# Kernel optimization log

Hardware: AMD Instinct MI355X
Metric: run time of the kernel (lower is better)

Reference implementation:

```python
import jax, jax.numpy as jnp
from jax import lax
import numpy as np

DN = ('NCHW', 'OIHW', 'NCHW')


def _conv(x, w, b, stride):
    y = lax.conv_general_dilated(x, w, (stride, stride), 'VALID', dimension_numbers=DN)
    return jax.nn.relu(y + b[None, :, None, None])


def setup_inputs() -> dict:
    key = jax.random.key(0)
    ks = jax.random.split(key, 24)
    B = 1024
    s = 0.05
    inp = {
        'rgb_image': jax.random.normal(ks[0], (B, 15000), jnp.float32),
        'distance': jax.random.uniform(ks[1], (B,), jnp.float32),
        'speed': jax.random.uniform(ks[2], (B,), jnp.float32),
        # LaneFollower (PilotNet-style CNN) params
        'conv1_w': s * jax.random.normal(ks[3], (24, 1, 5, 5), jnp.float32),
        'conv1_b': jnp.zeros((24,), jnp.float32),
        'conv2_w': s * jax.random.normal(ks[4], (36, 24, 5, 5), jnp.float32),
        'conv2_b': jnp.zeros((36,), jnp.float32),
        'conv3_w': s * jax.random.normal(ks[5], (48, 36, 5, 5), jnp.float32),
        'conv3_b': jnp.zeros((48,), jnp.float32),
        'conv4_w': s * jax.random.normal(ks[6], (64, 48, 3, 3), jnp.float32),
        'conv4_b': jnp.zeros((64,), jnp.float32),
        'fc1_w': s * jax.random.normal(ks[7], (5120, 100), jnp.float32),
        'fc1_b': jnp.zeros((100,), jnp.float32),
        'fc2_w': s * jax.random.normal(ks[8], (100, 50), jnp.float32),
        'fc2_b': jnp.zeros((50,), jnp.float32),
        'fc3_w': s * jax.random.normal(ks[9], (50, 10), jnp.float32),
        'fc3_b': jnp.zeros((10,), jnp.float32),
        'fc4_w': s * jax.random.normal(ks[10], (10, 1), jnp.float32),
        'fc4_b': jnp.zeros((1,), jnp.float32),
        # AEBS MLP params: 3 -> 12 -> 24 -> 4
        'a1_w': s * jax.random.normal(ks[11], (3, 12), jnp.float32),
        'a1_b': jnp.zeros((12,), jnp.float32),
        'a2_w': s * jax.random.normal(ks[12], (12, 24), jnp.float32),
        'a2_b': jnp.zeros((24,), jnp.float32),
        'a3_w': s * jax.random.normal(ks[13], (24, 4), jnp.float32),
        'a3_b': jnp.zeros((4,), jnp.float32),
    }
    return inp


def reference(rgb_image, distance, speed,
              conv1_w, conv1_b, conv2_w, conv2_b, conv3_w, conv3_b, conv4_w, conv4_b,
              fc1_w, fc1_b, fc2_w, fc2_b, fc3_w, fc3_b, fc4_w, fc4_b,
              a1_w, a1_b, a2_w, a2_b, a3_w, a3_b):
    B = rgb_image.shape[0]
    # lane_follow_input[i, j] = 1 if flat[i + j*200] > 0 else 0  ==> transpose of (75,200) reshape
    x = jnp.where(rgb_image.reshape(B, 75, 200) > 0, 1.0, 0.0).transpose(0, 2, 1)
    x = x[:, None, :, :]  # [B,1,200,75]
    x = _conv(x, conv1_w, conv1_b, 2)  # [B,24,98,36]
    x = _conv(x, conv2_w, conv2_b, 2)  # [B,36,47,16]
    x = _conv(x, conv3_w, conv3_b, 2)  # [B,48,22,6]
    x = _conv(x, conv4_w, conv4_b, 1)  # [B,64,20,4]
    x = x.reshape(B, -1)  # [B,5120]
    x = jax.nn.relu(x @ fc1_w + fc1_b)
    x = jax.nn.relu(x @ fc2_w + fc2_b)
    x = jax.nn.relu(x @ fc3_w + fc3_b)
    steering = (x @ fc4_w + fc4_b)[:, 0]  # [B]
    steering = lax.stop_gradient(steering)  # torch.no_grad() on lane follower
    aebs_in = jnp.stack([steering, distance, speed], axis=-1)  # [B,3]
    h = jax.nn.relu(aebs_in @ a1_w + a1_b)
    h = jax.nn.relu(h @ a2_w + a2_b)
    brake_force = h @ a3_w + a3_b  # [B,4]
    return brake_force
```

## Files before the change

### kernel.cpp

```cpp
#include <hip/hip_runtime.h>

typedef _Float16 f16;
typedef _Float16 f16x4 __attribute__((ext_vector_type(4)));
typedef _Float16 f16x8 __attribute__((ext_vector_type(8)));
typedef float f32x4 __attribute__((ext_vector_type(4)));

__global__ __launch_bounds__(256) void repack1m_k(f16* __restrict__ dst, const float* __restrict__ src){
  int idx = blockIdx.x*256 + threadIdx.x;
  if (idx >= 1024) return;
  int i = idx & 7, l = (idx >> 3) & 63, mt = idx >> 9;
  int co = mt*16 + (l & 15);
  int k = (l >> 4)*8 + i;
  f16 v = (f16)0.0f;
  if (co < 24 && k < 25){
    int kw = k / 5, kh = k - kw*5;
    v = (f16)src[co*25 + kh*5 + kw];
  }
  dst[idx] = v;
}
__global__ __launch_bounds__(256) void repack2c_k(f16* __restrict__ dst, const float* __restrict__ src){
  for (int idx = blockIdx.x*256 + threadIdx.x; idx < 29184; idx += gridDim.x*256){
    int i = idx & 7, l = (idx >> 3) & 63, rest = idx >> 9;
    int mt = rest % 3, s = rest / 3;
    int co = mt*16 + (l & 15);
    int k = s*32 + (l >> 4)*8 + i;
    f16 v = (f16)0.0f;
    if (co < 36 && k < 600){
      int tap = k / 24, ci = k - tap*24;
      v = (f16)src[(co*24 + ci)*25 + tap];
    }
    dst[idx] = v;
  }
}
__global__ __launch_bounds__(256) void repack3m_k(f16* __restrict__ dst, const float* __restrict__ src){
  for (int idx = blockIdx.x*256 + threadIdx.x; idx < 44544; idx += gridDim.x*256){
    int i = idx & 7, l = (idx >> 3) & 63, rest = idx >> 9;
    int mt = rest % 3, s = rest / 3;
    int co = mt*16 + (l & 15);
    f16 v = (f16)0.0f;
    if (s < 25){
      int ci = (l >> 4)*8 + i;
      v = (f16)src[(co*36 + ci)*25 + s];
    } else {
      int ke = (s - 25)*32 + (l >> 4)*8 + i;
      if (ke < 100){
        int p = ke >> 2, ci = 32 + (ke & 3);
        v = (f16)src[(co*36 + ci)*25 + p];
      }
    }
    dst[idx] = v;
  }
}
__global__ __launch_bounds__(256) void repack4m_k(f16* __restrict__ dst, const float* __restrict__ src){
  for (int idx = blockIdx.x*256 + threadIdx.x; idx < 28672; idx += gridDim.x*256){
    int i = idx & 7, l = (idx >> 3) & 63, rest = idx >> 9;
    int mt = rest & 3, s = rest >> 2;
    int co = mt*16 + (l & 15);
    int k = s*32 + (l >> 4)*8 + i;
    f16 v = (f16)0.0f;
    if (k < 432){
      int pos = k / 48, ci = k - pos*48;
      v = (f16)src[(co*48 + ci)*9 + pos];
    }
    dst[idx] = v;
  }
}
__global__ __launch_bounds__(256) void repackfc1_k(f16* __restrict__ dst, const float* __restrict__ src){
  for (int t = blockIdx.x*256 + threadIdx.x; t < 71680; t += gridDim.x*256){
    int l = t & 63, rest = t >> 6;
    int nt = rest % 7, s = rest / 7;
    int j = nt*16 + (l & 15);
    int kb = s*32 + (l >> 4)*8;
    union { f16 h[8]; f16x8 v; } pk;
    #pragma unroll
    for (int i=0;i<8;++i){
      int k = kb + i;
      int row = (k & 63)*80 + (k >> 6);
      pk.h[i] = (j < 100) ? (f16)src[(size_t)row*100 + j] : (f16)0.0f;
    }
    *(f16x8*)(dst + (size_t)t*8) = pk.v;
  }
}

__global__ __launch_bounds__(256) void conv12_k(const float* __restrict__ rgb, const f16* __restrict__ w1m,
                                                const float* __restrict__ b1, const f16* __restrict__ w2c,
                                                const float* __restrict__ b2, f16* __restrict__ a2, int ib){
  __shared__ __align__(16) f16 xb[75*44 + 8];
  __shared__ __align__(16) f16 xt[2*19*18*24];
  const int tid = threadIdx.x, bx = blockIdx.x;
  const int i = bx / 6, t = bx - i*6;
  const int h0 = t*32, oh0 = t*8;
  const float* img = rgb + (size_t)(ib + i)*15000;
  for (int idx = tid; idx < 825; idx += 256){
    int w = idx / 11, h4 = idx - w*11;
    int h = h0 + h4*4;
    union { f16 hv[4]; uint2 u; } pk;
    if (h < 200){
      float4 v = *(const float4*)(img + w*200 + h);
      pk.hv[0] = (v.x > 0.f) ? (f16)1.0f : (f16)0.0f;
      pk.hv[1] = (v.y > 0.f) ? (f16)1.0f : (f16)0.0f;
      pk.hv[2] = (v.z > 0.f) ? (f16)1.0f : (f16)0.0f;
      pk.hv[3] = (v.w > 0.f) ? (f16)1.0f : (f16)0.0f;
    } else {
      pk.u.x = 0u; pk.u.y = 0u;
    }
    *(uint2*)(xb + w*44 + h4*4) = pk.u;
  }
  __syncthreads();
  const int wv = tid >> 6, lane = tid & 63;
  const int jgrp = lane >> 4, npx = lane & 15;
  {
    f16x8 a1f0 = *(const f16x8*)(w1m + (size_t)lane*8);
    f16x8 a1f1 = *(const f16x8*)(w1m + (size_t)(64 + lane)*8);
    int koff[8];
    #pragma unroll
    for (int ii=0; ii<8; ++ii){
      int k = jgrp*8 + ii;
      if (k >= 25) k = 0;
      int kw = k / 5, kh = k - kw*5;
      koff[ii] = kw*44 + kh;
    }
    f32x4 bv0, bv1;
    #pragma unroll
    for (int reg=0; reg<4; ++reg){
      int c0 = jgrp*4 + reg;
      int c1 = 16 + jgrp*4 + reg;
      bv0[reg] = b1[c0];
      bv1[reg] = (c1 < 24) ? b1[c1] : 0.f;
    }
    for (int q=0; q<11; ++q){
      int nt = wv + 4*q;
      if (nt > 42) break;
      int pxt = nt*16 + npx;
      int px = (pxt > 683) ? 683 : pxt;
      int rr = px/36, ow = px - rr*36;
      const f16* gp = xb + 2*ow*44 + 2*rr;
      union { f16 h[8]; f16x8 v; } bq;
      #pragma unroll
      for (int ii=0; ii<8; ++ii) bq.h[ii] = gp[koff[ii]];
      f32x4 c0 = __builtin_amdgcn_mfma_f32_16x16x32_f16(a1f0, bq.v, bv0, 0, 0, 0);
      f32x4 c1 = __builtin_amdgcn_mfma_f32_16x16x32_f16(a1f1, bq.v, bv1, 0, 0, 0);
      if (pxt <= 683){
        f16* dst = xt + (((ow & 1)*19 + rr)*18 + (ow >> 1))*24;
        union { f16 h[4]; uint2 q2; } pk;
        #pragma unroll
        for (int reg=0; reg<4; ++reg){ float r = c0[reg]; if (r<0.f) r=0.f; pk.h[reg]=(f16)r; }
        *(uint2*)(dst + jgrp*4) = pk.q2;
        if (jgrp < 2){
          #pragma unroll
          for (int reg=0; reg<4; ++reg){ float r = c1[reg]; if (r<0.f) r=0.f; pk.h[reg]=(f16)r; }
          *(uint2*)(dst + 16 + jgrp*4) = pk.q2;
        }
      }
    }
  }
  __syncthreads();
  int baddr[19];
  #pragma unroll
  for (int s=0; s<19; ++s){
    int m = s*4 + jgrp;
    int tap = m / 3, r3 = m - tap*3;
    if (m >= 75){ tap = 24; r3 = 0; }
    int kh = tap / 5, kw = tap - kh*5;
    int par = kw & 1, kws = kw >> 1;
    baddr[s] = ((par*19 + kh)*18 + npx + kws)*24 + r3*8;
  }
  f32x4 acc2[3][2];
  #pragma unroll
  for (int mt=0; mt<3; ++mt){
    f32x4 bv;
    #pragma unroll
    for (int reg=0; reg<4; ++reg){
      int co = mt*16 + jgrp*4 + reg;
      bv[reg] = (co < 36) ? b2[co] : 0.0f;
    }
    acc2[mt][0] = bv; acc2[mt][1] = bv;
  }
  const f16* agl = w2c + (size_t)lane*8;
  const int rowo = 4*wv*432;
  #pragma unroll
  for (int s=0; s<19; ++s){
    f16x8 af[3];
    #pragma unroll
    for (int mt=0; mt<3; ++mt)
      af[mt] = *(const f16x8*)(agl + (size_t)(s*3 + mt)*512);
    const f16* bb0 = xt + baddr[s] + rowo;
    f16x8 bf[2];
    bf[0] = *(const f16x8*)(bb0);
    bf[1] = *(const f16x8*)(bb0 + 2*432);
    #pragma unroll
    for (int mt=0; mt<3; ++mt)
      #pragma unroll
      for (int u=0; u<2; ++u)
        acc2[mt][u] = __builtin_amdgcn_mfma_f32_16x16x32_f16(af[mt], bf[u], acc2[mt][u], 0, 0, 0);
  }
  #pragma unroll
  for (int u=0; u<2; ++u){
    const int oh = oh0 + 2*wv + u;
    if (oh >= 47) continue;
    #pragma unroll
    for (int mt=0; mt<3; ++mt){
      const int co0s = mt*16 + jgrp*4;
      if (co0s >= 36) continue;
      union { f16 h[4]; uint2 q; } pk;
      #pragma unroll
      for (int reg=0; reg<4; ++reg){
        float r = acc2[mt][u][reg]; if (r < 0.f) r = 0.f;
        pk.h[reg] = (f16)r;
      }
      *(uint2*)(a2 + (((size_t)i*47 + oh)*16 + npx)*36 + co0s) = pk.q;
    }
  }
}

__global__ __launch_bounds__(256) void conv34_k(const f16* __restrict__ a2, const f16* __restrict__ w3m,
                                                const float* __restrict__ b3, const f16* __restrict__ w4m,
                                                const float* __restrict__ b4, f16* __restrict__ a4){
  __shared__ __align__(16) f16 xt[27*680];
  __shared__ __align__(16) f16 a3t[12*6*56];
  const int tid = threadIdx.x, bx = blockIdx.x;
  const int i = bx >> 1, t = bx & 1;
  const int r0 = t*20, obase = t*10;
  {
    const uint2* s2 = (const uint2*)((const uint*)a2 + (size_t)i*13536);
    uint2* d = (uint2*)xt;
    for (int idx = tid; idx < 3888; idx += 256){
      int d2 = idx % 9, rc = idx / 9;
      int c = rc & 15, r = rc >> 4;
      int dwi = d2*2, jg = dwi >> 2, part = dwi & 3;
      d[(r*340 + jg*68 + c*4 + part) >> 1] = s2[((size_t)(r0 + r)*16 + c)*9 + d2];
    }
  }
  __syncthreads();
  const int wv = tid >> 6, lane = tid & 63;
  const int npx = lane & 15, jg = lane >> 4;
  {
    int baseq[2], ohl[2], owl[2];
    #pragma unroll
    for (int q=0;q<2;++q){
      int px = (wv*2+q)*16 + npx; if (px > 71) px = 71;
      ohl[q] = px/6; owl[q] = px - ohl[q]*6;
      baseq[q] = 2*ohl[q]*680 + jg*136 + 2*owl[q]*8;
    }
    f32x4 acc[3][2];
    #pragma unroll
    for (int mt=0;mt<3;++mt){
      f32x4 bv;
      #pragma unroll
      for (int reg=0;reg<4;++reg) bv[reg] = b3[mt*16 + jg*4 + reg];
      acc[mt][0]=bv; acc[mt][1]=bv;
    }
    const f16* agl = w3m + (size_t)lane*8;
    #pragma unroll 1
    for (int kh=0; kh<5; ++kh){
      #pragma unroll
      for (int kw=0; kw<5; ++kw){
        const int s = kh*5 + kw;
        f16x8 af[3];
        #pragma unroll
        for (int mt=0;mt<3;++mt)
          af[mt] = *(const f16x8*)(agl + (size_t)(s*3 + mt)*512);
        f16x8 bf[2];
        #pragma unroll
        for (int q=0;q<2;++q)
          bf[q] = *(const f16x8*)(xt + baseq[q] + kh*680 + kw*8);
        #pragma unroll
        for (int mt=0;mt<3;++mt)
          #pragma unroll
          for (int q=0;q<2;++q)
            acc[mt][q] = __builtin_amdgcn_mfma_f32_16x16x32_f16(af[mt], bf[q], acc[mt][q], 0, 0, 0);
      }
    }
    #pragma unroll
    for (int e=0;e<4;++e){
      const int s = 25 + e;
      f16x8 af[3];
      #pragma unroll
      for (int mt=0;mt<3;++mt)
        af[mt] = *(const f16x8*)(agl + (size_t)(s*3 + mt)*512);
      int p1 = e*8 + jg*2; int p2 = p1 + 1;
      if (p1 > 24) p1 = 24;
      if (p2 > 24) p2 = 24;
      const int kh1 = p1/5, kw1 = p1 - kh1*5;
      const int kh2 = p2/5, kw2 = p2 - kh2*5;
      #pragma unroll
      for (int q=0;q<2;++q){
        f16x4 lo = *(const f16x4*)(xt + (2*ohl[q]+kh1)*680 + 544 + (2*owl[q]+kw1)*8);
        f16x4 hi = *(const f16x4*)(xt + (2*ohl[q]+kh2)*680 + 544 + (2*owl[q]+kw2)*8);
        f16x8 bq = __builtin_shufflevector(lo, hi, 0,1,2,3,4,5,6,7);
        #pragma unroll
        for (int mt=0;mt<3;++mt)
          acc[mt][q] = __builtin_amdgcn_mfma_f32_16x16x32_f16(af[mt], bq, acc[mt][q], 0, 0, 0);
      }
    }
    #pragma unroll
    for (int q=0;q<2;++q){
      int px = (wv*2+q)*16 + npx;
      if (px >= 72) continue;
      #pragma unroll
      for (int mt=0;mt<3;++mt){
        union { f16 h[4]; uint2 q2; } pk;
        #pragma unroll
        for (int reg=0;reg<4;++reg){
          float r = acc[mt][q][reg]; if (r < 0.f) r = 0.f;
          pk.h[reg] = (f16)r;
        }
        *(uint2*)(a3t + px*56 + mt*16 + jg*4) = pk.q2;
      }
    }
  }
  __syncthreads();
  {
    f32x4 acc4[3];
    {
      f32x4 bv;
      #pragma unroll
      for (int reg=0;reg<4;++reg) bv[reg] = b4[wv*16 + jg*4 + reg];
      acc4[0]=bv; acc4[1]=bv; acc4[2]=bv;
    }
    int ohn[3], own[3];
    #pragma unroll
    for (int nt=0;nt<3;++nt){
      int px = nt*16 + npx; if (px > 39) px = 39;
      ohn[nt] = px >> 2; own[nt] = px & 3;
    }
    const f16* agl = w4m + (size_t)lane*8;
    #pragma unroll 1
    for (int s=0; s<14; ++s){
      f16x8 af = *(const f16x8*)(agl + (size_t)(s*4 + wv)*512);
      int k8 = s*32 + jg*8;
      int pos, ci0;
      if (k8 >= 432){ pos = 8; ci0 = 40; }
      else { pos = k8 / 48; ci0 = k8 - pos*48; }
      const int kh = pos/3, kw = pos - kh*3;
      #pragma unroll
      for (int nt=0;nt<3;++nt){
        const int r = ohn[nt] + kh, c = own[nt] + kw;
        f16x8 bq = *(const f16x8*)(a3t + (r*6 + c)*56 + ci0);
        acc4[nt] = __builtin_amdgcn_mfma_f32_16x16x32_f16(af, bq, acc4[nt], 0, 0, 0);
      }
    }
    #pragma unroll
    for (int nt=0;nt<3;++nt){
      int px = nt*16 + npx;
      if (px >= 40) continue;
      union { f16 h[4]; uint2 q2; } pk;
      #pragma unroll
      for (int reg=0;reg<4;++reg){
        float r = acc4[nt][reg]; if (r < 0.f) r = 0.f;
        pk.h[reg] = (f16)r;
      }
      *(uint2*)(a4 + ((size_t)i*80 + obase*4 + px)*64 + wv*16 + jg*4) = pk.q2;
    }
  }
}

__global__ __launch_bounds__(256) void fc1tail_k(const f16* __restrict__ a4, const f16* __restrict__ w1m,
    const float* __restrict__ fc1b, const float* __restrict__ dist, const float* __restrict__ speed,
    const float* __restrict__ fW2, const float* __restrict__ fb2,
    const float* __restrict__ fW3, const float* __restrict__ fb3,
    const float* __restrict__ fW4, const float* __restrict__ fb4,
    const float* __restrict__ aW1, const float* __restrict__ ab1,
    const float* __restrict__ aW2, const float* __restrict__ ab2,
    const float* __restrict__ aW3, const float* __restrict__ ab3,
    float* __restrict__ out, int ib){
  __shared__ float red[4][64][28];
  __shared__ float x1s[16][100];
  __shared__ float h2s[16][50];
  __shared__ float h3s[16][10];
  __shared__ float stg[16];
  __shared__ float hb1[16][12];
  __shared__ float hb2[16][24];
  const int tid = threadIdx.x;
  const int wv = tid >> 6, lane = tid & 63;
  const int img0 = blockIdx.x*16;
  f32x4 acc[7];
  #pragma unroll
  for (int nt=0;nt<7;++nt) acc[nt] = (f32x4){0.f,0.f,0.f,0.f};
  const f16* ap = a4 + (size_t)(img0 + (lane & 15))*5120 + (lane >> 4)*8;
  const f16* bp = w1m + (size_t)lane*8;
  #pragma unroll 1
  for (int s = wv*40; s < wv*40 + 40; ++s){
    f16x8 av = *(const f16x8*)(ap + s*32);
    #pragma unroll
    for (int nt=0;nt<7;++nt){
      f16x8 bv = *(const f16x8*)(bp + (size_t)(s*7 + nt)*512);
      acc[nt] = __builtin_amdgcn_mfma_f32_16x16x32_f16(av, bv, acc[nt], 0, 0, 0);
    }
  }
  #pragma unroll
  for (int nt=0;nt<7;++nt)
    #pragma unroll
    for (int reg=0;reg<4;++reg)
      red[wv][lane][nt*4+reg] = acc[nt][reg];
  __syncthreads();
  for (int idx = tid; idx < 1792; idx += 256){
    int imgl = idx / 112, j = idx - imgl*112;
    if (j >= 100) continue;
    int l = ((imgl >> 2) << 4) | (j & 15);
    int c = (j >> 4)*4 + (imgl & 3);
    float s = red[0][l][c] + red[1][l][c] + red[2][l][c] + red[3][l][c] + fc1b[j];
    x1s[imgl][j] = s > 0.f ? s : 0.f;
  }
  __syncthreads();
  const int g = tid >> 4, l16 = tid & 15;
  const int img = ib + img0 + g;
  for (int j = l16; j < 50; j += 16){
    float s = fb2[j];
    #pragma unroll 4
    for (int k = 0; k < 100; ++k) s = fmaf(x1s[g][k], fW2[k*50+j], s);
    h2s[g][j] = s > 0.f ? s : 0.f;
  }
  __syncthreads();
  if (l16 < 10){
    float s = fb3[l16];
    #pragma unroll
    for (int k = 0; k < 50; ++k) s = fmaf(h2s[g][k], fW3[k*10+l16], s);
    h3s[g][l16] = s > 0.f ? s : 0.f;
  }
  __syncthreads();
  if (l16 == 0){
    float s = fb4[0];
    #pragma unroll
    for (int k = 0; k < 10; ++k) s = fmaf(h3s[g][k], fW4[k], s);
    stg[g] = s;
  }
  __syncthreads();
  if (l16 < 12){
    float s0 = stg[g], dd = dist[img], sp = speed[img];
    float s = ab1[l16] + s0*aW1[l16] + dd*aW1[12+l16] + sp*aW1[24+l16];
    hb1[g][l16] = s > 0.f ? s : 0.f;
  }
  __syncthreads();
  for (int j = l16; j < 24; j += 16){
    float s = ab2[j];
    #pragma unroll
    for (int k=0;k<12;++k) s = fmaf(hb1[g][k], aW2[k*24+j], s);
    hb2[g][j] = s > 0.f ? s : 0.f;
  }
  __syncthreads();
  if (l16 < 4){
    float s = ab3[l16];
    #pragma unroll
    for (int k=0;k<24;++k) s = fmaf(hb2[g][k], aW3[k*4+l16], s);
    out[(size_t)img*4 + l16] = s;
  }
}

extern "C" void kernel_launch(void* const* d_in, const int* in_sizes, int n_in,
                              void* d_out, int out_size, void* d_ws, size_t ws_size,
                              hipStream_t stream){
  const float* rgb   = (const float*)d_in[0];
  const float* dist  = (const float*)d_in[1];
  const float* speed = (const float*)d_in[2];
  const float* cw1 = (const float*)d_in[3];
  const float* cb1 = (const float*)d_in[4];
  const float* cw2 = (const float*)d_in[5];
  const float* cb2 = (const float*)d_in[6];
  const float* cw3 = (const float*)d_in[7];
  const float* cb3 = (const float*)d_in[8];
  const float* cw4 = (const float*)d_in[9];
  const float* cb4 = (const float*)d_in[10];
  const float* fW1 = (const float*)d_in[11];
  const float* fb1 = (const float*)d_in[12];
  const float* fW2 = (const float*)d_in[13];
  const float* fb2 = (const float*)d_in[14];
  const float* fW3 = (const float*)d_in[15];
  const float* fb3 = (const float*)d_in[16];
  const float* fW4 = (const float*)d_in[17];
  const float* fb4 = (const float*)d_in[18];
  const float* aW1 = (const float*)d_in[19];
  const float* ab1 = (const float*)d_in[20];
  const float* aW2 = (const float*)d_in[21];
  const float* ab2 = (const float*)d_in[22];
  const float* aW3 = (const float*)d_in[23];
  const float* ab3 = (const float*)d_in[24];
  float* out = (float*)d_out;
  const int B = in_sizes[0] / 15000;

  auto ALN = [](size_t x){ return (x + 255) & ~(size_t)255; };
  const size_t fixed = ALN(2048) + ALN(58368) + ALN(89088) + ALN(57344) + ALN(1146880);

  int nc = 1;
  while (nc < 32){
    size_t Bc = (size_t)(B / nc);
    size_t need = fixed + ALN(Bc*54144) + ALN(Bc*10240);
    if (need <= ws_size) break;
    nc *= 2;
  }
  const int Bc = B / nc;

  char* ws = (char*)d_ws;
  size_t o = 0;
  auto alloc = [&](size_t bytes)->char*{ char* p = ws + o; o += ALN(bytes); return p; };
  f16* w1c = (f16*)alloc(2048);
  f16* w2c = (f16*)alloc(58368);
  f16* w3m = (f16*)alloc(89088);
  f16* w4m = (f16*)alloc(57344);
  f16* w1m = (f16*)alloc(1146880);
  f16* a2  = (f16*)alloc((size_t)Bc*54144);
  f16* a4  = (f16*)alloc((size_t)Bc*10240);

  repack1m_k<<<dim3(4),   dim3(256), 0, stream>>>(w1c, cw1);
  repack2c_k<<<dim3(114), dim3(256), 0, stream>>>(w2c, cw2);
  repack3m_k<<<dim3(174), dim3(256), 0, stream>>>(w3m, cw3);
  repack4m_k<<<dim3(112), dim3(256), 0, stream>>>(w4m, cw4);
  repackfc1_k<<<dim3(280), dim3(256), 0, stream>>>(w1m, fW1);

  for (int c = 0; c < nc; ++c){
    const int ib = c*Bc;
    conv12_k<<<dim3(Bc*6),   dim3(256), 0, stream>>>(rgb, w1c, cb1, w2c, cb2, a2, ib);
    conv34_k<<<dim3(Bc*2),   dim3(256), 0, stream>>>(a2, w3m, cb3, w4m, cb4, a4);
    fc1tail_k<<<dim3(Bc/16), dim3(256), 0, stream>>>(a4, w1m, fb1, dist, speed,
        fW2, fb2, fW3, fb3, fW4, fb4, aW1, ab1, aW2, ab2, aW3, ab3, out, ib);
  }
}
```

Before: 195.2 us.

## Merge weight repack kernels, pad conv1 LDS rows, halve fc1 tail block size

```diff
diff --git a/kernel.cpp b/kernel.cpp
--- a/kernel.cpp
+++ b/kernel.cpp
@@ -5,21 +5,24 @@
 typedef _Float16 f16x8 __attribute__((ext_vector_type(8)));
 typedef float f32x4 __attribute__((ext_vector_type(4)));
 
-__global__ __launch_bounds__(256) void repack1m_k(f16* __restrict__ dst, const float* __restrict__ src){
-  int idx = blockIdx.x*256 + threadIdx.x;
-  if (idx >= 1024) return;
-  int i = idx & 7, l = (idx >> 3) & 63, mt = idx >> 9;
-  int co = mt*16 + (l & 15);
-  int k = (l >> 4)*8 + i;
-  f16 v = (f16)0.0f;
-  if (co < 24 && k < 25){
-    int kw = k / 5, kh = k - kw*5;
-    v = (f16)src[co*25 + kh*5 + kw];
-  }
-  dst[idx] = v;
-}
-__global__ __launch_bounds__(256) void repack2c_k(f16* __restrict__ dst, const float* __restrict__ src){
-  for (int idx = blockIdx.x*256 + threadIdx.x; idx < 29184; idx += gridDim.x*256){
+__global__ __launch_bounds__(256) void repack_all_k(
+    f16* __restrict__ w1c, f16* __restrict__ w2c, f16* __restrict__ w3m,
+    f16* __restrict__ w4m, f16* __restrict__ wfc,
+    const float* __restrict__ s1, const float* __restrict__ s2, const float* __restrict__ s3,
+    const float* __restrict__ s4, const float* __restrict__ sf){
+  const int tid0 = blockIdx.x*256 + threadIdx.x, stride = gridDim.x*256;
+  for (int idx = tid0; idx < 1024; idx += stride){
+    int i = idx & 7, l = (idx >> 3) & 63, mt = idx >> 9;
+    int co = mt*16 + (l & 15);
+    int k = (l >> 4)*8 + i;
+    f16 v = (f16)0.0f;
+    if (co < 24 && k < 25){
+      int kw = k / 5, kh = k - kw*5;
+      v = (f16)s1[co*25 + kh*5 + kw];
+    }
+    w1c[idx] = v;
+  }
+  for (int idx = tid0; idx < 29184; idx += stride){
     int i = idx & 7, l = (idx >> 3) & 63, rest = idx >> 9;
     int mt = rest % 3, s = rest / 3;
     int co = mt*16 + (l & 15);
@@ -27,32 +30,28 @@
     f16 v = (f16)0.0f;
     if (co < 36 && k < 600){
       int tap = k / 24, ci = k - tap*24;
-      v = (f16)src[(co*24 + ci)*25 + tap];
-    }
-    dst[idx] = v;
-  }
-}
-__global__ __launch_bounds__(256) void repack3m_k(f16* __restrict__ dst, const float* __restrict__ src){
-  for (int idx = blockIdx.x*256 + threadIdx.x; idx < 44544; idx += gridDim.x*256){
+      v = (f16)s2[(co*24 + ci)*25 + tap];
+    }
+    w2c[idx] = v;
+  }
+  for (int idx = tid0; idx < 44544; idx += stride){
     int i = idx & 7, l = (idx >> 3) & 63, rest = idx >> 9;
     int mt = rest % 3, s = rest / 3;
     int co = mt*16 + (l & 15);
     f16 v = (f16)0.0f;
     if (s < 25){
       int ci = (l >> 4)*8 + i;
-      v = (f16)src[(co*36 + ci)*25 + s];
+      v = (f16)s3[(co*36 + ci)*25 + s];
     } else {
       int ke = (s - 25)*32 + (l >> 4)*8 + i;
       if (ke < 100){
         int p = ke >> 2, ci = 32 + (ke & 3);
-        v = (f16)src[(co*36 + ci)*25 + p];
-      }
-    }
-    dst[idx] = v;
-  }
-}
-__global__ __launch_bounds__(256) void repack4m_k(f16* __restrict__ dst, const float* __restrict__ src){
-  for (int idx = blockIdx.x*256 + threadIdx.x; idx < 28672; idx += gridDim.x*256){
+        v = (f16)s3[(co*36 + ci)*25 + p];
+      }
+    }
+    w3m[idx] = v;
+  }
+  for (int idx = tid0; idx < 28672; idx += stride){
     int i = idx & 7, l = (idx >> 3) & 63, rest = idx >> 9;
     int mt = rest & 3, s = rest >> 2;
     int co = mt*16 + (l & 15);
@@ -60,13 +59,11 @@
     f16 v = (f16)0.0f;
     if (k < 432){
       int pos = k / 48, ci = k - pos*48;
-      v = (f16)src[(co*48 + ci)*9 + pos];
-    }
-    dst[idx] = v;
-  }
-}
-__global__ __launch_bounds__(256) void repackfc1_k(f16* __restrict__ dst, const float* __restrict__ src){
-  for (int t = blockIdx.x*256 + threadIdx.x; t < 71680; t += gridDim.x*256){
+      v = (f16)s4[(co*48 + ci)*9 + pos];
+    }
+    w4m[idx] = v;
+  }
+  for (int t = tid0; t < 71680; t += stride){
     int l = t & 63, rest = t >> 6;
     int nt = rest % 7, s = rest / 7;
     int j = nt*16 + (l & 15);
@@ -76,35 +73,33 @@
     for (int i=0;i<8;++i){
       int k = kb + i;
       int row = (k & 63)*80 + (k >> 6);
-      pk.h[i] = (j < 100) ? (f16)src[(size_t)row*100 + j] : (f16)0.0f;
-    }
-    *(f16x8*)(dst + (size_t)t*8) = pk.v;
+      pk.h[i] = (j < 100) ? (f16)sf[(size_t)row*100 + j] : (f16)0.0f;
+    }
+    *(f16x8*)(wfc + (size_t)t*8) = pk.v;
   }
 }
 
 __global__ __launch_bounds__(256) void conv12_k(const float* __restrict__ rgb, const f16* __restrict__ w1m,
                                                 const float* __restrict__ b1, const f16* __restrict__ w2c,
                                                 const float* __restrict__ b2, f16* __restrict__ a2, int ib){
-  __shared__ __align__(16) f16 xb[75*44 + 8];
+  __shared__ __align__(16) f16 xb[75*46 + 8];
   __shared__ __align__(16) f16 xt[2*19*18*24];
   const int tid = threadIdx.x, bx = blockIdx.x;
   const int i = bx / 6, t = bx - i*6;
   const int h0 = t*32, oh0 = t*8;
   const float* img = rgb + (size_t)(ib + i)*15000;
-  for (int idx = tid; idx < 825; idx += 256){
-    int w = idx / 11, h4 = idx - w*11;
-    int h = h0 + h4*4;
-    union { f16 hv[4]; uint2 u; } pk;
+  for (int idx = tid; idx < 1575; idx += 256){
+    int w = idx / 21, t2 = idx - w*21;
+    int hh = 2*t2, h = h0 + hh;
+    union { f16 hv[2]; uint u; } pk;
     if (h < 200){
-      float4 v = *(const float4*)(img + w*200 + h);
+      float2 v = *(const float2*)(img + w*200 + h);
       pk.hv[0] = (v.x > 0.f) ? (f16)1.0f : (f16)0.0f;
       pk.hv[1] = (v.y > 0.f) ? (f16)1.0f : (f16)0.0f;
-      pk.hv[2] = (v.z > 0.f) ? (f16)1.0f : (f16)0.0f;
-      pk.hv[3] = (v.w > 0.f) ? (f16)1.0f : (f16)0.0f;
     } else {
-      pk.u.x = 0u; pk.u.y = 0u;
-    }
-    *(uint2*)(xb + w*44 + h4*4) = pk.u;
+      pk.u = 0u;
+    }
+    *(uint*)(xb + w*46 + hh) = pk.u;
   }
   __syncthreads();
   const int wv = tid >> 6, lane = tid & 63;
@@ -118,7 +113,7 @@
       int k = jgrp*8 + ii;
       if (k >= 25) k = 0;
       int kw = k / 5, kh = k - kw*5;
-      koff[ii] = kw*44 + kh;
+      koff[ii] = kw*46 + kh;
     }
     f32x4 bv0, bv1;
     #pragma unroll
@@ -134,7 +129,7 @@
       int pxt = nt*16 + npx;
       int px = (pxt > 683) ? 683 : pxt;
       int rr = px/36, ow = px - rr*36;
-      const f16* gp = xb + 2*ow*44 + 2*rr;
+      const f16* gp = xb + 2*(ow*46 + rr);
       union { f16 h[8]; f16x8 v; } bq;
       #pragma unroll
       for (int ii=0; ii<8; ++ii) bq.h[ii] = gp[koff[ii]];
@@ -363,21 +358,23 @@
     const float* __restrict__ aW1, const float* __restrict__ ab1,
     const float* __restrict__ aW2, const float* __restrict__ ab2,
     const float* __restrict__ aW3, const float* __restrict__ ab3,
-    float* __restrict__ out, int ib){
+    float* __restrict__ out, int ib, int n){
   __shared__ float red[4][64][28];
-  __shared__ float x1s[16][100];
-  __shared__ float h2s[16][50];
-  __shared__ float h3s[16][10];
-  __shared__ float stg[16];
-  __shared__ float hb1[16][12];
-  __shared__ float hb2[16][24];
+  __shared__ float x1s[8][100];
+  __shared__ float h2s[8][50];
+  __shared__ float h3s[8][10];
+  __shared__ float stg[8];
+  __shared__ float hb1[8][12];
+  __shared__ float hb2[8][24];
   const int tid = threadIdx.x;
   const int wv = tid >> 6, lane = tid & 63;
-  const int img0 = blockIdx.x*16;
+  const int img0 = blockIdx.x*8;
   f32x4 acc[7];
   #pragma unroll
   for (int nt=0;nt<7;++nt) acc[nt] = (f32x4){0.f,0.f,0.f,0.f};
-  const f16* ap = a4 + (size_t)(img0 + (lane & 15))*5120 + (lane >> 4)*8;
+  int ia = img0 + (lane & 15);
+  if (ia > n-1) ia = n-1;
+  const f16* ap = a4 + (size_t)ia*5120 + (lane >> 4)*8;
   const f16* bp = w1m + (size_t)lane*8;
   #pragma unroll 1
   for (int s = wv*40; s < wv*40 + 40; ++s){
@@ -394,7 +391,7 @@
     for (int reg=0;reg<4;++reg)
       red[wv][lane][nt*4+reg] = acc[nt][reg];
   __syncthreads();
-  for (int idx = tid; idx < 1792; idx += 256){
+  for (int idx = tid; idx < 896; idx += 256){
     int imgl = idx / 112, j = idx - imgl*112;
     if (j >= 100) continue;
     int l = ((imgl >> 2) << 4) | (j & 15);
@@ -403,47 +400,47 @@
     x1s[imgl][j] = s > 0.f ? s : 0.f;
   }
   __syncthreads();
-  const int g = tid >> 4, l16 = tid & 15;
+  const int g = tid >> 5, l32 = tid & 31;
   const int img = ib + img0 + g;
-  for (int j = l16; j < 50; j += 16){
+  for (int j = l32; j < 50; j += 32){
     float s = fb2[j];
     #pragma unroll 4
     for (int k = 0; k < 100; ++k) s = fmaf(x1s[g][k], fW2[k*50+j], s);
     h2s[g][j] = s > 0.f ? s : 0.f;
   }
   __syncthreads();
-  if (l16 < 10){
-    float s = fb3[l16];
-    #pragma unroll
-    for (int k = 0; k < 50; ++k) s = fmaf(h2s[g][k], fW3[k*10+l16], s);
-    h3s[g][l16] = s > 0.f ? s : 0.f;
-  }
-  __syncthreads();
-  if (l16 == 0){
+  if (l32 < 10){
+    float s = fb3[l32];
+    #pragma unroll
+    for (int k = 0; k < 50; ++k) s = fmaf(h2s[g][k], fW3[k*10+l32], s);
+    h3s[g][l32] = s > 0.f ? s : 0.f;
+  }
+  __syncthreads();
+  if (l32 == 0){
     float s = fb4[0];
     #pragma unroll
     for (int k = 0; k < 10; ++k) s = fmaf(h3s[g][k], fW4[k], s);
     stg[g] = s;
   }
   __syncthreads();
-  if (l16 < 12){
+  if (l32 < 12){
     float s0 = stg[g], dd = dist[img], sp = speed[img];
-    float s = ab1[l16] + s0*aW1[l16] + dd*aW1[12+l16] + sp*aW1[24+l16];
-    hb1[g][l16] = s > 0.f ? s : 0.f;
-  }
-  __syncthreads();
-  for (int j = l16; j < 24; j += 16){
-    float s = ab2[j];
-    #pragma unroll
-    for (int k=0;k<12;++k) s = fmaf(hb1[g][k], aW2[k*24+j], s);
-    hb2[g][j] = s > 0.f ? s : 0.f;
-  }
-  __syncthreads();
-  if (l16 < 4){
-    float s = ab3[l16];
-    #pragma unroll
-    for (int k=0;k<24;++k) s = fmaf(hb2[g][k], aW3[k*4+l16], s);
-    out[(size_t)img*4 + l16] = s;
+    float s = ab1[l32] + s0*aW1[l32] + dd*aW1[12+l32] + sp*aW1[24+l32];
+    hb1[g][l32] = s > 0.f ? s : 0.f;
+  }
+  __syncthreads();
+  if (l32 < 24){
+    float s = ab2[l32];
+    #pragma unroll
+    for (int k=0;k<12;++k) s = fmaf(hb1[g][k], aW2[k*24+l32], s);
+    hb2[g][l32] = s > 0.f ? s : 0.f;
+  }
+  __syncthreads();
+  if (l32 < 4){
+    float s = ab3[l32];
+    #pragma unroll
+    for (int k=0;k<24;++k) s = fmaf(hb2[g][k], aW3[k*4+l32], s);
+    out[(size_t)img*4 + l32] = s;
   }
 }
 
@@ -501,17 +498,14 @@
   f16* a2  = (f16*)alloc((size_t)Bc*54144);
   f16* a4  = (f16*)alloc((size_t)Bc*10240);
 
-  repack1m_k<<<dim3(4),   dim3(256), 0, stream>>>(w1c, cw1);
-  repack2c_k<<<dim3(114), dim3(256), 0, stream>>>(w2c, cw2);
-  repack3m_k<<<dim3(174), dim3(256), 0, stream>>>(w3m, cw3);
-  repack4m_k<<<dim3(112), dim3(256), 0, stream>>>(w4m, cw4);
-  repackfc1_k<<<dim3(280), dim3(256), 0, stream>>>(w1m, fW1);
+  repack_all_k<<<dim3(280), dim3(256), 0, stream>>>(w1c, w2c, w3m, w4m, w1m,
+                                                    cw1, cw2, cw3, cw4, fW1);
 
   for (int c = 0; c < nc; ++c){
     const int ib = c*Bc;
-    conv12_k<<<dim3(Bc*6),   dim3(256), 0, stream>>>(rgb, w1c, cb1, w2c, cb2, a2, ib);
-    conv34_k<<<dim3(Bc*2),   dim3(256), 0, stream>>>(a2, w3m, cb3, w4m, cb4, a4);
-    fc1tail_k<<<dim3(Bc/16), dim3(256), 0, stream>>>(a4, w1m, fb1, dist, speed,
-        fW2, fb2, fW3, fb3, fW4, fb4, aW1, ab1, aW2, ab2, aW3, ab3, out, ib);
+    conv12_k<<<dim3(Bc*6),  dim3(256), 0, stream>>>(rgb, w1c, cb1, w2c, cb2, a2, ib);
+    conv34_k<<<dim3(Bc*2),  dim3(256), 0, stream>>>(a2, w3m, cb3, w4m, cb4, a4);
+    fc1tail_k<<<dim3(Bc/8), dim3(256), 0, stream>>>(a4, w1m, fb1, dist, speed,
+        fW2, fb2, fW3, fb3, fW4, fb4, aW1, ab1, aW2, ab2, aW3, ab3, out, ib, Bc);
   }
 }
```

New measurement: 184.7 us. -5.4%, faster.
